# Kernel optimization log

Hardware: AMD Instinct MI355X
Metric: run time of the kernel (lower is better)

## Reference

```python
import jax, jax.numpy as jnp
import numpy as np

DIM = 512
HEADS = 8
DIM_HEAD = 64
HIDDEN = HEADS * DIM_HEAD  # 512
SCALE = DIM_HEAD ** -0.5


def setup_inputs() -> dict:
    key = jax.random.key(0)
    k1, k2, k3, k4 = jax.random.split(key, 4)
    B, N = 8, 4096
    x = jax.random.normal(k1, (B, DIM, N), dtype=jnp.float32)
    # Conv1d with kernel_size=1, no bias -> weight [out, in]
    w_qkv = jax.random.normal(k2, (HIDDEN * 3, DIM), dtype=jnp.float32) * (DIM ** -0.5)
    w_out = jax.random.normal(k3, (DIM, HIDDEN), dtype=jnp.float32) * (HIDDEN ** -0.5)
    b_out = jax.random.normal(k4, (DIM,), dtype=jnp.float32) * 0.01
    return {"x": x, "w_qkv": w_qkv, "w_out": w_out, "b_out": b_out}


def reference(x, w_qkv, w_out, b_out):
    B, _, N = x.shape
    # pointwise conv1d == channel GEMM: [3*hidden, dim] x [b, dim, n]
    qkv = jnp.einsum('oi,bin->bon', w_qkv, x)
    q, k, v = jnp.split(qkv, 3, axis=1)
    # b (h c) n -> b h c n
    reshape = lambda t: t.reshape(B, HEADS, DIM_HEAD, N)
    q, k, v = reshape(q), reshape(k), reshape(v)
    q = q * SCALE
    k = jax.nn.softmax(k, axis=-1)  # softmax over sequence dim n
    # context: [b h d e] = sum_n k[b h d n] v[b h e n]
    context = jnp.einsum('bhdn,bhen->bhde', k, v)
    # out: [b h e n] = sum_d context[b h d e] q[b h d n]
    out = jnp.einsum('bhde,bhdn->bhen', context, q)
    out = out.reshape(B, HIDDEN, N)  # b (h e) n
    return jnp.einsum('oi,bin->bon', w_out, out) + b_out[None, :, None]
```

## Files before the change

### kernel.cpp

```cpp
#include <hip/hip_runtime.h>
#include <hip/hip_bf16.h>
#include <cstdint>

typedef unsigned short u16;
typedef __attribute__((ext_vector_type(8))) short bf16x8;
typedef __attribute__((ext_vector_type(4))) float f32x4;

__device__ __forceinline__ u16 f2b(float f) {
  union { float f; unsigned u; } x; x.f = f;
  unsigned r = x.u + 0x7fffu + ((x.u >> 16) & 1u);
  return (u16)(r >> 16);
}
__device__ __forceinline__ float b2f(u16 u) {
  union { unsigned u; float f; } x; x.u = ((unsigned)u) << 16;
  return x.f;
}
__device__ __forceinline__ void gld16(void* lds, const void* g) {
  __builtin_amdgcn_global_load_lds((const __attribute__((address_space(1))) void*)g,
                                   (__attribute__((address_space(3))) void*)lds, 16, 0, 0);
}
__device__ __forceinline__ int sw_idx(int n, int c) {
  return n * 64 + ((((c >> 2) ^ (n >> 2)) & 15) << 2) + (c & 3);
}

__global__ __launch_bounds__(256) void prep(const float* __restrict__ w_qkv,
                                            u16* __restrict__ wkv,
                                            u16* __restrict__ wqT,
                                            float* __restrict__ zbuf) {
  const int tid = threadIdx.x;
  const int blk = blockIdx.x;
  if (blk < 512) {
    const int i = blk * 1024 + tid * 4;
    const float4 v = *(const float4*)(w_qkv + 262144 + i);
    ushort4 r; r.x = f2b(v.x); r.y = f2b(v.y); r.z = f2b(v.z); r.w = f2b(v.w);
    *(ushort4*)(wkv + i) = r;
  } else if (blk < 576) {
    __shared__ u16 t[4096];
    const int bb = blk - 512;
    const int i0 = (bb & 7) * 64;
    const int c0 = (bb >> 3) * 64;
    const int il = (tid & 15) * 4;
    const int cl = tid >> 4;
#pragma unroll
    for (int r = 0; r < 4; r++) {
      const int c = cl + r * 16;
      const float4 v = *(const float4*)(w_qkv + (c0 + c) * 512 + i0 + il);
      t[sw_idx(il + 0, c)] = f2b(v.x);
      t[sw_idx(il + 1, c)] = f2b(v.y);
      t[sw_idx(il + 2, c)] = f2b(v.z);
      t[sw_idx(il + 3, c)] = f2b(v.w);
    }
    __syncthreads();
    const int cw = (tid & 15) * 4;
#pragma unroll
    for (int r = 0; r < 4; r++) {
      const int i = cl + r * 16;
      const u16* tp = &t[sw_idx(i, cw)];
      ushort4 o; o.x = tp[0]; o.y = tp[1]; o.z = tp[2]; o.w = tp[3];
      *(ushort4*)(wqT + (i0 + i) * 512 + c0 + cw) = o;
    }
  } else {
    const int zi = (blk - 576) * 1024 + tid * 4;
    if (zi < 266240) *(float4*)(zbuf + zi) = float4{0.f, 0.f, 0.f, 0.f};
  }
}

__global__ __launch_bounds__(256) void xt_kern(const float* __restrict__ x,
                                               u16* __restrict__ xt) {
  __shared__ u16 t[4096];
  const int tid = threadIdx.x;
  const int b = blockIdx.z;
  const int n0 = blockIdx.x * 64;
  const int c0 = blockIdx.y * 64;
  const int nl = (tid & 15) * 4;
  const int cl = tid >> 4;
#pragma unroll
  for (int r = 0; r < 4; r++) {
    const int c = cl + r * 16;
    const float4 v = *(const float4*)(x + ((long)b * 512 + c0 + c) * 4096 + n0 + nl);
    t[sw_idx(nl + 0, c)] = f2b(v.x);
    t[sw_idx(nl + 1, c)] = f2b(v.y);
    t[sw_idx(nl + 2, c)] = f2b(v.z);
    t[sw_idx(nl + 3, c)] = f2b(v.w);
  }
  __syncthreads();
  const int cw = (tid & 15) * 4;
#pragma unroll
  for (int r = 0; r < 4; r++) {
    const int n = cl + r * 16;
    const u16* tp = &t[sw_idx(n, cw)];
    ushort4 o; o.x = tp[0]; o.y = tp[1]; o.z = tp[2]; o.w = tp[3];
    *(ushort4*)(xt + ((long)b * 4096 + n0 + n) * 512 + c0 + cw) = o;
  }
}

__global__ __launch_bounds__(256) void kv_gemm(const u16* __restrict__ wkv,
                                               const u16* __restrict__ xt,
                                               u16* __restrict__ kv,
                                               float* __restrict__ rsum) {
  __shared__ u16 As[128 * 32];
  __shared__ u16 Bs[128 * 32];
  const int tid = threadIdx.x;
  const int wid = tid >> 6;
  const int lane = tid & 63;
  const int wm = wid >> 1, wn = wid & 1;
  const int gn = blockIdx.x, gm = blockIdx.y, b = blockIdx.z;

  const u16* Ab = wkv + (long)gm * 128 * 512;
  const u16* Bb = xt + ((long)b * 4096 + (long)gn * 128) * 512;

  f32x4 acc[4][4] = {};
  const int q8 = (lane >> 4) * 8;
  const int mr = lane & 15;

  for (int kk = 0; kk < 512; kk += 32) {
    __syncthreads();
#pragma unroll
    for (int i = 0; i < 2; i++) {
      const int slot = i * 256 + tid;
      const int row = slot >> 2;
      const int kc = (slot & 3) * 8;
      gld16((char*)As + i * 4096 + wid * 1024, Ab + (long)row * 512 + kk + kc);
      gld16((char*)Bs + i * 4096 + wid * 1024, Bb + (long)row * 512 + kk + kc);
    }
    __syncthreads();
    bf16x8 af[4], bfv[4];
#pragma unroll
    for (int i = 0; i < 4; i++)
      af[i] = *(const bf16x8*)(As + (wm * 64 + i * 16 + mr) * 32 + q8);
#pragma unroll
    for (int j = 0; j < 4; j++)
      bfv[j] = *(const bf16x8*)(Bs + (wn * 64 + j * 16 + mr) * 32 + q8);
#pragma unroll
    for (int i = 0; i < 4; i++)
#pragma unroll
      for (int j = 0; j < 4; j++)
        acc[i][j] = __builtin_amdgcn_mfma_f32_16x16x32_bf16(af[i], bfv[j], acc[i][j], 0, 0, 0);
  }

  const int quad = lane >> 4;
  const bool isK = (gm < 4);
  u16* outb = kv + (long)b * 1024 * 4096;
#pragma unroll
  for (int i = 0; i < 4; i++) {
#pragma unroll
    for (int r = 0; r < 4; r++) {
      const int grow = gm * 128 + wm * 64 + i * 16 + quad * 4 + r;
      u16* rowp = outb + (long)grow * 4096 + gn * 128 + wn * 64 + mr;
      float s = 0.f;
#pragma unroll
      for (int j = 0; j < 4; j++) {
        float v = acc[i][j][r];
        if (isK) v = __expf(v);
        const u16 bv = f2b(v);
        rowp[j * 16] = bv;
        if (isK) s += b2f(bv);
      }
      if (isK) {
        s += __shfl_xor(s, 1);
        s += __shfl_xor(s, 2);
        s += __shfl_xor(s, 4);
        s += __shfl_xor(s, 8);
        if (mr == 0) atomicAdd(rsum + b * 512 + grow, s);
      }
    }
  }
}

__global__ __launch_bounds__(256) void ctx_gemm(const u16* __restrict__ kv,
                                                float* __restrict__ ctx) {
  __shared__ u16 Es[64 * 64];
  __shared__ u16 Vs[64 * 64];
  const int tid = threadIdx.x;
  const int wid = tid >> 6;
  const int lane = tid & 63;
  const int wm = wid >> 1, wn = wid & 1;
  const int bh = blockIdx.x, kc = blockIdx.y;
  const int b = bh >> 3, h = bh & 7;

  const u16* Eg = kv + ((long)b * 1024 + h * 64) * 4096 + kc * 512;
  const u16* Vg = kv + ((long)b * 1024 + 512 + h * 64) * 4096 + kc * 512;

  const int mr = lane & 15;
  const int quad = lane >> 4;
  const int q8 = quad * 8;

  f32x4 acc[2][2] = {};

  for (int nn = 0; nn < 512; nn += 64) {
    __syncthreads();
#pragma unroll
    for (int c = 0; c < 2; c++) {
      const int off = c * 4096 + wid * 1024 + lane * 16;
      const int row = off >> 7;
      const int cu = (off & 127) >> 1;
      gld16((char*)Es + c * 4096 + wid * 1024, Eg + (long)row * 4096 + nn + cu);
      gld16((char*)Vs + c * 4096 + wid * 1024, Vg + (long)row * 4096 + nn + cu);
    }
    __syncthreads();
#pragma unroll
    for (int ks = 0; ks < 2; ks++) {
      bf16x8 ef[2], vf[2];
#pragma unroll
      for (int ii = 0; ii < 2; ii++)
        ef[ii] = *(const bf16x8*)(Es + (wm * 32 + ii * 16 + mr) * 64 + ks * 32 + q8);
#pragma unroll
      for (int jj = 0; jj < 2; jj++)
        vf[jj] = *(const bf16x8*)(Vs + (wn * 32 + jj * 16 + mr) * 64 + ks * 32 + q8);
#pragma unroll
      for (int ii = 0; ii < 2; ii++)
#pragma unroll
        for (int jj = 0; jj < 2; jj++)
          acc[ii][jj] = __builtin_amdgcn_mfma_f32_16x16x32_bf16(ef[ii], vf[jj], acc[ii][jj], 0, 0, 0);
    }
  }

  float* cb = ctx + (long)bh * 4096;
#pragma unroll
  for (int ii = 0; ii < 2; ii++)
#pragma unroll
    for (int jj = 0; jj < 2; jj++)
#pragma unroll
      for (int r = 0; r < 4; r++) {
        const int d = wm * 32 + ii * 16 + quad * 4 + r;
        const int e = wn * 32 + jj * 16 + mr;
        atomicAdd(cb + d * 64 + e, acc[ii][jj][r]);
      }
}

__global__ __launch_bounds__(256) void wc_kern(const float* __restrict__ ctxp,
                                               const float* __restrict__ rsump,
                                               const float* __restrict__ wout,
                                               u16* __restrict__ Wc) {
  __shared__ float cs[64 * 65];
  const int tid = threadIdx.x;
  const int bh = blockIdx.x, og = blockIdx.y;
  const int b = bh >> 3, h = bh & 7;
  for (int i = tid; i < 4096; i += 256) {
    const int d = i >> 6, e = i & 63;
    cs[e * 65 + d] = ctxp[(long)bh * 4096 + i] / rsump[(long)bh * 64 + d];
  }
  __syncthreads();
  const int d = tid & 63;
  const int o0 = og * 128 + (tid >> 6) * 32;
  float csr[64];
#pragma unroll
  for (int e = 0; e < 64; e++) csr[e] = cs[e * 65 + d];
  u16* wcp = Wc + (long)b * 512 * 512;
  for (int rr = 0; rr < 32; rr++) {
    const int o = o0 + rr;
    const float* wrow = wout + (long)o * 512 + h * 64;
    float a0 = 0.f, a1 = 0.f, a2 = 0.f, a3 = 0.f;
#pragma unroll
    for (int e = 0; e < 64; e += 4) {
      a0 += wrow[e + 0] * csr[e + 0];
      a1 += wrow[e + 1] * csr[e + 1];
      a2 += wrow[e + 2] * csr[e + 2];
      a3 += wrow[e + 3] * csr[e + 3];
    }
    wcp[(long)o * 512 + h * 64 + d] = f2b((a0 + a1) + (a2 + a3));
  }
}

__global__ __launch_bounds__(256) void weff_gemm(const u16* __restrict__ Wc,
                                                 const u16* __restrict__ wqT,
                                                 u16* __restrict__ Weff) {
  __shared__ u16 As[128 * 32];
  __shared__ u16 Bs[128 * 32];
  const int tid = threadIdx.x;
  const int wid = tid >> 6;
  const int lane = tid & 63;
  const int wm = wid >> 1, wn = wid & 1;
  const int gn = blockIdx.x, gm = blockIdx.y, b = blockIdx.z;

  const u16* Ab = Wc + (long)b * 512 * 512 + (long)gm * 128 * 512;
  const u16* Bb = wqT + (long)gn * 128 * 512;

  f32x4 acc[4][4] = {};
  const int q8 = (lane >> 4) * 8;
  const int mr = lane & 15;

  for (int kk = 0; kk < 512; kk += 32) {
    __syncthreads();
#pragma unroll
    for (int i = 0; i < 2; i++) {
      const int slot = i * 256 + tid;
      const int row = slot >> 2;
      const int kc = (slot & 3) * 8;
      gld16((char*)As + i * 4096 + wid * 1024, Ab + (long)row * 512 + kk + kc);
      gld16((char*)Bs + i * 4096 + wid * 1024, Bb + (long)row * 512 + kk + kc);
    }
    __syncthreads();
    bf16x8 af[4], bfv[4];
#pragma unroll
    for (int i = 0; i < 4; i++)
      af[i] = *(const bf16x8*)(As + (wm * 64 + i * 16 + mr) * 32 + q8);
#pragma unroll
    for (int j = 0; j < 4; j++)
      bfv[j] = *(const bf16x8*)(Bs + (wn * 64 + j * 16 + mr) * 32 + q8);
#pragma unroll
    for (int i = 0; i < 4; i++)
#pragma unroll
      for (int j = 0; j < 4; j++)
        acc[i][j] = __builtin_amdgcn_mfma_f32_16x16x32_bf16(af[i], bfv[j], acc[i][j], 0, 0, 0);
  }

  const int col = lane & 15;
  const int quad = lane >> 4;
  u16* wb = Weff + (long)b * 512 * 512;
#pragma unroll
  for (int i = 0; i < 4; i++)
#pragma unroll
    for (int r = 0; r < 4; r++) {
      const int grow = gm * 128 + wm * 64 + i * 16 + quad * 4 + r;
#pragma unroll
      for (int j = 0; j < 4; j++) {
        const int gcol = gn * 128 + wn * 64 + j * 16 + col;
        wb[(long)grow * 512 + gcol] = f2b(acc[i][j][r] * 0.125f);
      }
    }
}

__global__ __launch_bounds__(256) void out_gemm(const u16* __restrict__ Weff,
                                                const u16* __restrict__ xt,
                                                const float* __restrict__ bias,
                                                float* __restrict__ outp) {
  __shared__ u16 As[128 * 32];
  __shared__ u16 Bs[128 * 32];
  const int tid = threadIdx.x;
  const int wid = tid >> 6;
  const int lane = tid & 63;
  const int wm = wid >> 1, wn = wid & 1;
  const int gn = blockIdx.x, gm = blockIdx.y, b = blockIdx.z;

  const u16* Ab = Weff + (long)b * 512 * 512 + (long)gm * 128 * 512;
  const u16* Bb = xt + ((long)b * 4096 + (long)gn * 128) * 512;

  f32x4 acc[4][4] = {};
  const int q8 = (lane >> 4) * 8;
  const int mr = lane & 15;

  for (int kk = 0; kk < 512; kk += 32) {
    __syncthreads();
#pragma unroll
    for (int i = 0; i < 2; i++) {
      const int slot = i * 256 + tid;
      const int row = slot >> 2;
      const int kc = (slot & 3) * 8;
      gld16((char*)As + i * 4096 + wid * 1024, Ab + (long)row * 512 + kk + kc);
      gld16((char*)Bs + i * 4096 + wid * 1024, Bb + (long)row * 512 + kk + kc);
    }
    __syncthreads();
    bf16x8 af[4], bfv[4];
#pragma unroll
    for (int i = 0; i < 4; i++)
      af[i] = *(const bf16x8*)(As + (wm * 64 + i * 16 + mr) * 32 + q8);
#pragma unroll
    for (int j = 0; j < 4; j++)
      bfv[j] = *(const bf16x8*)(Bs + (wn * 64 + j * 16 + mr) * 32 + q8);
#pragma unroll
    for (int i = 0; i < 4; i++)
#pragma unroll
      for (int j = 0; j < 4; j++)
        acc[i][j] = __builtin_amdgcn_mfma_f32_16x16x32_bf16(af[i], bfv[j], acc[i][j], 0, 0, 0);
  }

  const int col = lane & 15;
  const int quad = lane >> 4;
#pragma unroll
  for (int i = 0; i < 4; i++)
#pragma unroll
    for (int r = 0; r < 4; r++) {
      const int grow = gm * 128 + wm * 64 + i * 16 + quad * 4 + r;
      const float bv = bias[grow];
#pragma unroll
      for (int j = 0; j < 4; j++) {
        const long gcol = (long)gn * 128 + wn * 64 + j * 16 + col;
        outp[((long)b * 512 + grow) * 4096 + gcol] = acc[i][j][r] + bv;
      }
    }
}

extern "C" void kernel_launch(void* const* d_in, const int* in_sizes, int n_in,
                              void* d_out, int out_size, void* d_ws, size_t ws_size,
                              hipStream_t stream) {
  const float* x = (const float*)d_in[0];
  const float* w_qkv = (const float*)d_in[1];
  const float* w_out = (const float*)d_in[2];
  const float* b_out = (const float*)d_in[3];
  float* out = (float*)d_out;
  char* ws = (char*)d_ws;

  u16* xt = (u16*)(ws + 0);
  u16* kv = (u16*)(ws + 33554432);
  u16* wkv = (u16*)(ws + 100663296);
  u16* wqT = (u16*)(ws + 101711872);
  u16* wc = (u16*)(ws + 102236160);
  u16* weff = (u16*)(ws + 106430464);
  float* ctx = (float*)(ws + 110624768);
  float* rsum = (float*)(ws + 111673344);

  prep<<<836, 256, 0, stream>>>(w_qkv, wkv, wqT, ctx);
  xt_kern<<<dim3(64, 8, 8), 256, 0, stream>>>(x, xt);
  kv_gemm<<<dim3(32, 8, 8), 256, 0, stream>>>(wkv, xt, kv, rsum);
  ctx_gemm<<<dim3(64, 8), 256, 0, stream>>>(kv, ctx);
  wc_kern<<<dim3(64, 4), 256, 0, stream>>>(ctx, rsum, w_out, wc);
  weff_gemm<<<dim3(4, 4, 8), 256, 0, stream>>>(wc, wqT, weff);
  out_gemm<<<dim3(32, 4, 8), 256, 0, stream>>>(weff, xt, b_out, out);
}
```

Before: 273.1 us.

## Fuse K/V projection GEMM with context GEMM to avoid KV round trip

Fuses the K/V projection GEMM and the context GEMM into one kernel. The weight rows are reordered per head so each block computes a head's K and V tiles for 256 sequence positions and keeps exp(K) and V in swizzled shared memory. The context product is then accumulated directly, with atomics into ctx. This removes the 64MB bf16 KV intermediate write and read plus one launch, but cuts the grid from 2048 to 1024 blocks and adds extra shared memory and syncs per block.

```diff
diff --git a/kernel.cpp b/kernel.cpp
--- a/kernel.cpp
+++ b/kernel.cpp
@@ -22,18 +22,25 @@
 __device__ __forceinline__ int sw_idx(int n, int c) {
   return n * 64 + ((((c >> 2) ^ (n >> 2)) & 15) << 2) + (c & 3);
 }
+__device__ __forceinline__ int ekb(int row, int c2) {
+  return (row * 256 + c2) ^ ((((row >> 3) ^ row) & 7) << 4);
+}
 
 __global__ __launch_bounds__(256) void prep(const float* __restrict__ w_qkv,
-                                            u16* __restrict__ wkv,
+                                            u16* __restrict__ wkvh,
                                             u16* __restrict__ wqT,
                                             float* __restrict__ zbuf) {
   const int tid = threadIdx.x;
   const int blk = blockIdx.x;
   if (blk < 512) {
     const int i = blk * 1024 + tid * 4;
+    const int ri = i >> 9;
+    const int col = i & 511;
+    const int h = (ri >> 6) & 7;
+    const int orow = h * 128 + ((ri >> 9) << 6) + (ri & 63);
     const float4 v = *(const float4*)(w_qkv + 262144 + i);
     ushort4 r; r.x = f2b(v.x); r.y = f2b(v.y); r.z = f2b(v.z); r.w = f2b(v.w);
-    *(ushort4*)(wkv + i) = r;
+    *(ushort4*)(wkvh + orow * 512 + col) = r;
   } else if (blk < 576) {
     __shared__ u16 t[4096];
     const int bb = blk - 512;
@@ -94,124 +101,103 @@
   }
 }
 
-__global__ __launch_bounds__(256) void kv_gemm(const u16* __restrict__ wkv,
-                                               const u16* __restrict__ xt,
-                                               u16* __restrict__ kv,
-                                               float* __restrict__ rsum) {
+__global__ __launch_bounds__(256) void kvctx(const u16* __restrict__ wkvh,
+                                             const u16* __restrict__ xt,
+                                             float* __restrict__ ctx,
+                                             float* __restrict__ rsum) {
   __shared__ u16 As[128 * 32];
   __shared__ u16 Bs[128 * 32];
+  __shared__ u16 Ek[64 * 128];
+  __shared__ u16 Vs[64 * 128];
   const int tid = threadIdx.x;
   const int wid = tid >> 6;
   const int lane = tid & 63;
   const int wm = wid >> 1, wn = wid & 1;
-  const int gn = blockIdx.x, gm = blockIdx.y, b = blockIdx.z;
-
-  const u16* Ab = wkv + (long)gm * 128 * 512;
-  const u16* Bb = xt + ((long)b * 4096 + (long)gn * 128) * 512;
-
-  f32x4 acc[4][4] = {};
+  const int nc = blockIdx.x, h = blockIdx.y, b = blockIdx.z;
+  const int bh = b * 8 + h;
+
+  const u16* Ab = wkvh + (long)h * 128 * 512;
   const int q8 = (lane >> 4) * 8;
   const int mr = lane & 15;
-
-  for (int kk = 0; kk < 512; kk += 32) {
-    __syncthreads();
-#pragma unroll
-    for (int i = 0; i < 2; i++) {
-      const int slot = i * 256 + tid;
-      const int row = slot >> 2;
-      const int kc = (slot & 3) * 8;
-      gld16((char*)As + i * 4096 + wid * 1024, Ab + (long)row * 512 + kk + kc);
-      gld16((char*)Bs + i * 4096 + wid * 1024, Bb + (long)row * 512 + kk + kc);
-    }
-    __syncthreads();
-    bf16x8 af[4], bfv[4];
-#pragma unroll
-    for (int i = 0; i < 4; i++)
-      af[i] = *(const bf16x8*)(As + (wm * 64 + i * 16 + mr) * 32 + q8);
-#pragma unroll
-    for (int j = 0; j < 4; j++)
-      bfv[j] = *(const bf16x8*)(Bs + (wn * 64 + j * 16 + mr) * 32 + q8);
-#pragma unroll
-    for (int i = 0; i < 4; i++)
+  const int quad = lane >> 4;
+
+  f32x4 acc2[2][2] = {};
+
+  for (int s = 0; s < 2; s++) {
+    const long nbase = (long)nc * 256 + s * 128;
+    const u16* Bb = xt + ((long)b * 4096 + nbase) * 512;
+    f32x4 acc[4][4] = {};
+
+    for (int kk = 0; kk < 512; kk += 32) {
+      __syncthreads();
+#pragma unroll
+      for (int i = 0; i < 2; i++) {
+        const int slot = i * 256 + tid;
+        const int row = slot >> 2;
+        const int kc = (slot & 3) * 8;
+        gld16((char*)As + i * 4096 + wid * 1024, Ab + (long)row * 512 + kk + kc);
+        gld16((char*)Bs + i * 4096 + wid * 1024, Bb + (long)row * 512 + kk + kc);
+      }
+      __syncthreads();
+      bf16x8 af[4], bfv[4];
+#pragma unroll
+      for (int i = 0; i < 4; i++)
+        af[i] = *(const bf16x8*)(As + (wm * 64 + i * 16 + mr) * 32 + q8);
 #pragma unroll
       for (int j = 0; j < 4; j++)
-        acc[i][j] = __builtin_amdgcn_mfma_f32_16x16x32_bf16(af[i], bfv[j], acc[i][j], 0, 0, 0);
-  }
-
-  const int quad = lane >> 4;
-  const bool isK = (gm < 4);
-  u16* outb = kv + (long)b * 1024 * 4096;
-#pragma unroll
-  for (int i = 0; i < 4; i++) {
-#pragma unroll
-    for (int r = 0; r < 4; r++) {
-      const int grow = gm * 128 + wm * 64 + i * 16 + quad * 4 + r;
-      u16* rowp = outb + (long)grow * 4096 + gn * 128 + wn * 64 + mr;
-      float s = 0.f;
-#pragma unroll
-      for (int j = 0; j < 4; j++) {
-        float v = acc[i][j][r];
-        if (isK) v = __expf(v);
-        const u16 bv = f2b(v);
-        rowp[j * 16] = bv;
-        if (isK) s += b2f(bv);
-      }
-      if (isK) {
-        s += __shfl_xor(s, 1);
-        s += __shfl_xor(s, 2);
-        s += __shfl_xor(s, 4);
-        s += __shfl_xor(s, 8);
-        if (mr == 0) atomicAdd(rsum + b * 512 + grow, s);
-      }
-    }
-  }
-}
-
-__global__ __launch_bounds__(256) void ctx_gemm(const u16* __restrict__ kv,
-                                                float* __restrict__ ctx) {
-  __shared__ u16 Es[64 * 64];
-  __shared__ u16 Vs[64 * 64];
-  const int tid = threadIdx.x;
-  const int wid = tid >> 6;
-  const int lane = tid & 63;
-  const int wm = wid >> 1, wn = wid & 1;
-  const int bh = blockIdx.x, kc = blockIdx.y;
-  const int b = bh >> 3, h = bh & 7;
-
-  const u16* Eg = kv + ((long)b * 1024 + h * 64) * 4096 + kc * 512;
-  const u16* Vg = kv + ((long)b * 1024 + 512 + h * 64) * 4096 + kc * 512;
-
-  const int mr = lane & 15;
-  const int quad = lane >> 4;
-  const int q8 = quad * 8;
-
-  f32x4 acc[2][2] = {};
-
-  for (int nn = 0; nn < 512; nn += 64) {
-    __syncthreads();
-#pragma unroll
-    for (int c = 0; c < 2; c++) {
-      const int off = c * 4096 + wid * 1024 + lane * 16;
-      const int row = off >> 7;
-      const int cu = (off & 127) >> 1;
-      gld16((char*)Es + c * 4096 + wid * 1024, Eg + (long)row * 4096 + nn + cu);
-      gld16((char*)Vs + c * 4096 + wid * 1024, Vg + (long)row * 4096 + nn + cu);
-    }
-    __syncthreads();
-#pragma unroll
-    for (int ks = 0; ks < 2; ks++) {
+        bfv[j] = *(const bf16x8*)(Bs + (wn * 64 + j * 16 + mr) * 32 + q8);
+#pragma unroll
+      for (int i = 0; i < 4; i++)
+#pragma unroll
+        for (int j = 0; j < 4; j++)
+          acc[i][j] = __builtin_amdgcn_mfma_f32_16x16x32_bf16(af[i], bfv[j], acc[i][j], 0, 0, 0);
+    }
+
+    u16* dst = (wm == 0) ? Ek : Vs;
+#pragma unroll
+    for (int i = 0; i < 4; i++) {
+#pragma unroll
+      for (int r = 0; r < 4; r++) {
+        const int row = i * 16 + quad * 4 + r;
+        float sloc = 0.f;
+#pragma unroll
+        for (int j = 0; j < 4; j++) {
+          float v = acc[i][j][r];
+          if (wm == 0) v = __expf(v);
+          const u16 bv = f2b(v);
+          const int col = wn * 64 + j * 16 + mr;
+          *(u16*)((char*)dst + ekb(row, col * 2)) = bv;
+          if (wm == 0) sloc += b2f(bv);
+        }
+        if (wm == 0) {
+          sloc += __shfl_xor(sloc, 1);
+          sloc += __shfl_xor(sloc, 2);
+          sloc += __shfl_xor(sloc, 4);
+          sloc += __shfl_xor(sloc, 8);
+          if (mr == 0) atomicAdd(rsum + (long)bh * 64 + row, sloc);
+        }
+      }
+    }
+    __syncthreads();
+
+#pragma unroll
+    for (int ks = 0; ks < 4; ks++) {
       bf16x8 ef[2], vf[2];
 #pragma unroll
+      for (int ii = 0; ii < 2; ii++) {
+        const int row = wm * 32 + ii * 16 + mr;
+        ef[ii] = *(const bf16x8*)((const char*)Ek + ekb(row, (ks * 32 + q8) * 2));
+      }
+#pragma unroll
+      for (int jj = 0; jj < 2; jj++) {
+        const int row = wn * 32 + jj * 16 + mr;
+        vf[jj] = *(const bf16x8*)((const char*)Vs + ekb(row, (ks * 32 + q8) * 2));
+      }
+#pragma unroll
       for (int ii = 0; ii < 2; ii++)
-        ef[ii] = *(const bf16x8*)(Es + (wm * 32 + ii * 16 + mr) * 64 + ks * 32 + q8);
-#pragma unroll
-      for (int jj = 0; jj < 2; jj++)
-        vf[jj] = *(const bf16x8*)(Vs + (wn * 32 + jj * 16 + mr) * 64 + ks * 32 + q8);
-#pragma unroll
-      for (int ii = 0; ii < 2; ii++)
 #pragma unroll
         for (int jj = 0; jj < 2; jj++)
-          acc[ii][jj] = __builtin_amdgcn_mfma_f32_16x16x32_bf16(ef[ii], vf[jj], acc[ii][jj], 0, 0, 0);
+          acc2[ii][jj] = __builtin_amdgcn_mfma_f32_16x16x32_bf16(ef[ii], vf[jj], acc2[ii][jj], 0, 0, 0);
     }
   }
 
@@ -224,7 +210,7 @@
       for (int r = 0; r < 4; r++) {
         const int d = wm * 32 + ii * 16 + quad * 4 + r;
         const int e = wn * 32 + jj * 16 + mr;
-        atomicAdd(cb + d * 64 + e, acc[ii][jj][r]);
+        atomicAdd(cb + d * 64 + e, acc2[ii][jj][r]);
       }
 }
 
@@ -392,18 +378,16 @@
   char* ws = (char*)d_ws;
 
   u16* xt = (u16*)(ws + 0);
-  u16* kv = (u16*)(ws + 33554432);
-  u16* wkv = (u16*)(ws + 100663296);
-  u16* wqT = (u16*)(ws + 101711872);
-  u16* wc = (u16*)(ws + 102236160);
-  u16* weff = (u16*)(ws + 106430464);
-  float* ctx = (float*)(ws + 110624768);
-  float* rsum = (float*)(ws + 111673344);
-
-  prep<<<836, 256, 0, stream>>>(w_qkv, wkv, wqT, ctx);
+  u16* wkvh = (u16*)(ws + 33554432);
+  u16* wqT = (u16*)(ws + 34603008);
+  u16* wc = (u16*)(ws + 35127296);
+  u16* weff = (u16*)(ws + 39321600);
+  float* ctx = (float*)(ws + 43515904);
+  float* rsum = (float*)(ws + 44564480);
+
+  prep<<<836, 256, 0, stream>>>(w_qkv, wkvh, wqT, ctx);
   xt_kern<<<dim3(64, 8, 8), 256, 0, stream>>>(x, xt);
-  kv_gemm<<<dim3(32, 8, 8), 256, 0, stream>>>(wkv, xt, kv, rsum);
-  ctx_gemm<<<dim3(64, 8), 256, 0, stream>>>(kv, ctx);
+  kvctx<<<dim3(16, 8, 8), 256, 0, stream>>>(wkvh, xt, ctx, rsum);
   wc_kern<<<dim3(64, 4), 256, 0, stream>>>(ctx, rsum, w_out, wc);
   weff_gemm<<<dim3(4, 4, 8), 256, 0, stream>>>(wc, wqT, weff);
   out_gemm<<<dim3(32, 4, 8), 256, 0, stream>>>(weff, xt, b_out, out);
```

Result: slower. 318.3 us (+16.6%).
